# Kernel optimization log

Measured on AMD Instinct MI355X. Metric: run time of the kernel, lower is better.

The kernel has to match this reference:

```python
import jax, jax.numpy as jnp
import numpy as np

DIM = 256
HEADS = 8
DIM_HEAD = 32
AGENT = 6
WIN = 7


def _relative_position_index(L, Wh, Ww):
    coords = np.stack(np.meshgrid(np.arange(L), np.arange(Wh), np.arange(Ww), indexing='ij'))
    cf = coords.reshape(3, -1)                      # (3, N)
    rel = cf[:, :, None] - cf[:, None, :]           # (3, N, N)
    rel = rel.transpose(1, 2, 0).astype(np.int64)   # (N, N, 3)
    rel[..., 0] += L - 1
    rel[..., 1] += Wh - 1
    rel[..., 2] += Ww - 1
    rel[..., 0] *= (2 * Wh - 1) * (2 * Ww - 1)
    rel[..., 1] *= 2 * Ww - 1
    return rel.sum(-1)                              # (N, N)


def setup_inputs() -> dict:
    key = jax.random.key(0)
    k1, k2, k3, k4, k5 = jax.random.split(key, 5)
    B, X, Y = 2, 8, 8
    x = jax.random.normal(k1, (B, AGENT, X, Y, WIN, WIN, DIM), dtype=jnp.float32)
    mask = jax.random.randint(k2, (B, X, Y, WIN, WIN, 1, AGENT), 0, 2, dtype=jnp.int32)
    w_qkv = jax.random.normal(k3, (3 * DIM, DIM), dtype=jnp.float32) * 0.02
    w_out = jax.random.normal(k4, (DIM, DIM), dtype=jnp.float32) * 0.02
    n_bias = (2 * AGENT - 1) * (2 * WIN - 1) * (2 * WIN - 1)
    bias_table = jax.random.normal(k5, (n_bias, HEADS), dtype=jnp.float32) * 0.02
    return {"x": x, "mask": mask, "w_qkv": w_qkv, "w_out": w_out, "bias_table": bias_table}


def reference(x, mask, w_qkv, w_out, bias_table):
    B, L, X, Y, W1, W2, C = x.shape
    h, dh = HEADS, DIM_HEAD
    N = L * W1 * W2
    scale = dh ** -0.5

    # 'b l x y w1 w2 d -> (b x y) (l w1 w2) d'
    xr = jnp.transpose(x, (0, 2, 3, 1, 4, 5, 6)).reshape(B * X * Y, N, C)

    qkv = jnp.einsum('bnc,ec->bne', xr, w_qkv)      # (Bw, N, 3C)
    q, k, v = jnp.split(qkv, 3, axis=-1)
    def to_heads(t):
        return jnp.transpose(t.reshape(B * X * Y, N, h, dh), (0, 2, 1, 3))
    q, k, v = to_heads(q) * scale, to_heads(k), to_heads(v)

    sim = jnp.einsum('bhid,bhjd->bhij', q, k)       # (Bw, h, N, N)

    rel_idx = jnp.asarray(_relative_position_index(L, W1, W2))
    bias = bias_table[rel_idx]                      # (N, N, h)
    sim = sim + jnp.transpose(bias, (2, 0, 1))[None]

    # 'b x y w1 w2 e l -> (b x y) e (l w1 w2)'
    m = jnp.transpose(mask, (0, 1, 2, 5, 6, 3, 4)).reshape(B * X * Y, 1, N)
    sim = jnp.where(m[:, :, None, :] == 0, jnp.float32(-1e9), sim)

    attn = jax.nn.softmax(sim, axis=-1)
    out = jnp.einsum('bhij,bhjd->bhid', attn, v)    # (Bw, h, N, dh)

    # 'b h (l w1 w2) d -> b l w1 w2 (h d)'
    out = jnp.transpose(out, (0, 2, 1, 3)).reshape(B * X * Y, L, W1, W2, C)
    out = jnp.einsum('blwvc,ec->blwve', out, w_out)

    # '(b x y) l w1 w2 d -> b l x y w1 w2 d'
    out = out.reshape(B, X, Y, L, W1, W2, C)
    return jnp.transpose(out, (0, 3, 1, 2, 4, 5, 6))
```

## Files before the change

### kernel.cpp

```cpp
#include <hip/hip_runtime.h>
#include <hip/hip_bf16.h>

#define DIM 256
#define HEADS 8
#define DH 32
#define AGENT 6
#define WIN 7
#define NTOK 294
#define BWIN 128
#define SCALE 0.17677669529663687f
#define LOG2E 1.4426950408889634f
#define TP 19
#define QSTR 40
#define PSTR 320

typedef __hip_bfloat16 bf16;
typedef __attribute__((ext_vector_type(8))) short s16x8;
typedef __attribute__((ext_vector_type(4))) float f32x4;
typedef __attribute__((ext_vector_type(4))) unsigned int u32x4;

#if __has_builtin(__builtin_amdgcn_exp2f)
#define EXP2(x) __builtin_amdgcn_exp2f(x)
#else
#define EXP2(x) exp2f(x)
#endif

__device__ __forceinline__ float bfv(unsigned short u){ return __uint_as_float(((unsigned int)u) << 16); }
__device__ __forceinline__ unsigned short f2bu(float f){
    bf16 b = __float2bfloat16(f); return *reinterpret_cast<unsigned short*>(&b);
}
__device__ __forceinline__ float rdf(const void* p, size_t idx, int isf32) {
    return isf32 ? ((const float*)p)[idx] : bfv(((const unsigned short*)p)[idx]);
}

__device__ __forceinline__ int vtswz(int d, int cByte) {
    return (d * (PSTR * 2) + cByte) ^ (((d >> 1) & 7) << 4);
}

__device__ __forceinline__ void gll16(const void* gp, void* lp) {
    __builtin_amdgcn_global_load_lds(
        (const __attribute__((address_space(1))) unsigned int*)gp,
        (__attribute__((address_space(3))) unsigned int*)lp, 16, 0, 0);
}

__device__ __forceinline__ int detect_flag(const unsigned short* __restrict__ xraw,
                                           int* sflag, int nthreads) {
    if (threadIdx.x == 0) *sflag = 0;
    __syncthreads();
    int bad = 0;
    for (int i = threadIdx.x; i < 8192; i += nthreads) {
        float v = bfv(xraw[i]);
        if (!(fabsf(v) <= 1e10f)) bad = 1;
    }
    if (bad) atomicOr(sflag, 1);
    __syncthreads();
    return *sflag;
}

__global__ __launch_bounds__(256) void prep_kernel(
    const unsigned short* __restrict__ xraw,
    const void* __restrict__ wq, const void* __restrict__ wo, const void* __restrict__ bt,
    unsigned short* __restrict__ Wq, unsigned short* __restrict__ Wo,
    unsigned short* __restrict__ biasB) {
    __shared__ int sflag;
    const int isf32 = detect_flag(xraw, &sflag, 256);
    const int bid = blockIdx.x;
    if (bid < 722) {
        int idx = bid * 256 + threadIdx.x;
        int lane = idx & 63; int t = idx >> 6;
        int jt = t % TP; t /= TP; int it = t % TP; int h = t / TP;
        int i = it * 16 + (lane & 15);
        int g = lane >> 4;
        ushort4 v;
        unsigned short* vp = (unsigned short*)&v;
        #pragma unroll
        for (int r = 0; r < 4; r++) {
            int j = jt * 16 + g * 4 + r;
            float val = 0.f;
            if (i < NTOK && j < NTOK) {
                int li = i / 49, ri = i - li * 49, w1i = ri / 7, w2i = ri - w1i * 7;
                int lj = j / 49, rj = j - lj * 49, w1j = rj / 7, w2j = rj - w1j * 7;
                int rel = (li - lj + AGENT - 1) * 169 + (w1i - w1j + WIN - 1) * 13 + (w2i - w2j + WIN - 1);
                val = rdf(bt, (size_t)rel * HEADS + h, isf32) * LOG2E;
            }
            vp[r] = f2bu(val);
        }
        ((ushort4*)biasB)[idx] = v;
    } else {
        int c = (bid - 722) * 256 + threadIdx.x;
        const void* src; unsigned short* dst; size_t off;
        if (c < 24576) { src = wq; dst = Wq; off = (size_t)c * 8; }
        else           { src = wo; dst = Wo; off = (size_t)(c - 24576) * 8; }
        if (isf32) {
            const float4* s4 = (const float4*)((const float*)src + off);
            float4 v0 = s4[0], v1 = s4[1];
            s16x8 u;
            u[0] = (short)f2bu(v0.x); u[1] = (short)f2bu(v0.y); u[2] = (short)f2bu(v0.z); u[3] = (short)f2bu(v0.w);
            u[4] = (short)f2bu(v1.x); u[5] = (short)f2bu(v1.y); u[6] = (short)f2bu(v1.z); u[7] = (short)f2bu(v1.w);
            *(s16x8*)(dst + off) = u;
        } else {
            *(uint4*)(dst + off) = *(const uint4*)((const unsigned short*)src + off);
        }
    }
}

__device__ __forceinline__ void stage64_g(const unsigned short* __restrict__ g,
                                          unsigned short* lds, size_t rowBase) {
    const int lane = threadIdx.x & 63, wv = threadIdx.x >> 6;
    const int sub = lane >> 5;
    const int colB = (lane & 31) << 4;
    #pragma unroll
    for (int k = 0; k < 8; k++) {
        const int rr = (wv * 8 + k) * 2 + sub;
        const int cg = colB ^ ((rr & 7) << 4);
        gll16((const char*)g + (rowBase + (size_t)rr) * 512 + cg,
              lds + (size_t)(wv * 8 + k) * 512);
    }
}

__device__ __forceinline__ void stage64_f(const float* __restrict__ g,
                                          unsigned short* lds, size_t rowBase) {
    const int tid = threadIdx.x;
    #pragma unroll
    for (int k = 0; k < 8; k++) {
        int ch = k * 256 + tid;
        int rr = ch >> 5;
        int cB = (ch & 31) << 4;
        int cg = cB ^ ((rr & 7) << 4);
        const f32x4* s4 = (const f32x4*)(g + (rowBase + (size_t)rr) * 256 + (cg >> 1));
        f32x4 v0 = __builtin_nontemporal_load(s4);
        f32x4 v1 = __builtin_nontemporal_load(s4 + 1);
        s16x8 u;
        u[0] = (short)f2bu(v0[0]); u[1] = (short)f2bu(v0[1]); u[2] = (short)f2bu(v0[2]); u[3] = (short)f2bu(v0[3]);
        u[4] = (short)f2bu(v1[0]); u[5] = (short)f2bu(v1[1]); u[6] = (short)f2bu(v1[2]); u[7] = (short)f2bu(v1[3]);
        *(s16x8*)(lds + (size_t)rr * 256 + (cB >> 1)) = u;
    }
}

__global__ __launch_bounds__(256) void qkv_mfma(
    const void* __restrict__ xin, const unsigned short* __restrict__ Wq,
    bf16* __restrict__ Q, bf16* __restrict__ K, bf16* __restrict__ V) {
    __shared__ unsigned short As[64 * 256];
    __shared__ unsigned short Bs[64 * 256];
    __shared__ int sflag;
    const int isf32 = detect_flag((const unsigned short*)xin, &sflag, 256);
    const size_t mBase = (size_t)blockIdx.x * 64;
    if (isf32) stage64_f((const float*)xin, As, mBase);
    else       stage64_g((const unsigned short*)xin, As, mBase);
    const int tid = threadIdx.x;
    const int wave = tid >> 6, lane = tid & 63;
    const int li = lane & 15, g = lane >> 4;
    const int wm = wave & 1, wn = wave >> 1;
    unsigned int rowOff[2][4];
    #pragma unroll
    for (int mi = 0; mi < 2; mi++)
        #pragma unroll
        for (int r = 0; r < 4; r++) {
            unsigned int m = (unsigned int)mBase + wm * 32 + mi * 16 + g * 4 + r;
            unsigned int w2 = m % 7u, t1 = m / 7u;
            unsigned int w1 = t1 % 7u, t2 = t1 / 7u;
            unsigned int yy = t2 & 7u, t3 = t2 >> 3;
            unsigned int xx = t3 & 7u, t4 = t3 >> 3;
            unsigned int l = t4 % 6u, b = t4 / 6u;
            unsigned int bw = (b << 6) | (xx << 3) | yy;
            unsigned int n = l * 49u + w1 * 7u + w2;
            rowOff[mi][r] = bw * 75264u + n * 32u;
        }
    const int koX = (li & 7) * 8;
    for (int pc = 0; pc < 12; pc++) {
        __syncthreads();
        stage64_g(Wq, Bs, (size_t)pc * 64);
        __syncthreads();
        f32x4 acc[2][2];
        #pragma unroll
        for (int mi = 0; mi < 2; mi++)
            #pragma unroll
            for (int ni = 0; ni < 2; ni++) acc[mi][ni] = (f32x4){0.f, 0.f, 0.f, 0.f};
        #pragma unroll
        for (int kc = 0; kc < 8; kc++) {
            const int ko = (kc * 32 + g * 8) ^ koX;
            s16x8 a0 = *(const s16x8*)&As[(wm * 32 + li) * 256 + ko];
            s16x8 a1 = *(const s16x8*)&As[(wm * 32 + 16 + li) * 256 + ko];
            s16x8 b0 = *(const s16x8*)&Bs[(wn * 32 + li) * 256 + ko];
            s16x8 b1 = *(const s16x8*)&Bs[(wn * 32 + 16 + li) * 256 + ko];
            acc[0][0] = __builtin_amdgcn_mfma_f32_16x16x32_bf16(a0, b0, acc[0][0], 0, 0, 0);
            acc[0][1] = __builtin_amdgcn_mfma_f32_16x16x32_bf16(a0, b1, acc[0][1], 0, 0, 0);
            acc[1][0] = __builtin_amdgcn_mfma_f32_16x16x32_bf16(a1, b0, acc[1][0], 0, 0, 0);
            acc[1][1] = __builtin_amdgcn_mfma_f32_16x16x32_bf16(a1, b1, acc[1][1], 0, 0, 0);
        }
        const int p = pc >> 2;
        bf16* dst = (p == 0) ? Q : (p == 1) ? K : V;
        const float sc = (p == 0) ? (SCALE * LOG2E) : 1.0f;
        const unsigned int hoff = ((pc & 3) * 2 + wn) * 9408u;
        #pragma unroll
        for (int ni = 0; ni < 2; ni++) {
            const unsigned int d = ni * 16 + li;
            #pragma unroll
            for (int mi = 0; mi < 2; mi++)
                #pragma unroll
                for (int r = 0; r < 4; r++)
                    dst[(size_t)(rowOff[mi][r] + hoff + d)] =
                        __float2bfloat16(acc[mi][ni][r] * sc);
        }
    }
}

__global__ __launch_bounds__(512, 2) void attn_mfma(
    const bf16* __restrict__ Q, const bf16* __restrict__ K, const bf16* __restrict__ V,
    const unsigned short* __restrict__ biasB, const int* __restrict__ mask,
    bf16* __restrict__ AT) {
    __shared__ unsigned short Qs[304 * QSTR];
    __shared__ unsigned short Ks[304 * QSTR];
    __shared__ unsigned short Vt[32 * PSTR];
    __shared__ int ms[320];
    const int tid = threadIdx.x;
    const int bw = blockIdx.x >> 3, h = blockIdx.x & 7;
    const size_t base = ((size_t)bw * HEADS + h) * NTOK * DH;
    const unsigned int* Qg = (const unsigned int*)(Q + base);
    const unsigned int* Kg = (const unsigned int*)(K + base);
    const unsigned int* Vg = (const unsigned int*)(V + base);
    char* VtB = (char*)Vt;
    for (int gg = tid; gg < NTOK * DH / 2; gg += 512) {
        int r = gg >> 4, d2 = (gg & 15) * 2;
        unsigned int uq = __builtin_nontemporal_load(&Qg[gg]);
        unsigned int uk = __builtin_nontemporal_load(&Kg[gg]);
        unsigned int uv = __builtin_nontemporal_load(&Vg[gg]);
        *(unsigned int*)&Qs[r * QSTR + d2] = uq;
        *(unsigned int*)&Ks[r * QSTR + d2] = uk;
        *(unsigned short*)(VtB + vtswz(d2,     r * 2)) = (unsigned short)(uv & 0xffffu);
        *(unsigned short*)(VtB + vtswz(d2 + 1, r * 2)) = (unsigned short)(uv >> 16);
    }
    for (int e = NTOK * QSTR + tid; e < 304 * QSTR; e += 512) { Qs[e] = 0; Ks[e] = 0; }
    for (int idx = tid; idx < 32 * (PSTR - NTOK); idx += 512) {
        int d = idx / (PSTR - NTOK), c = NTOK + idx % (PSTR - NTOK);
        *(unsigned short*)(VtB + vtswz(d, c * 2)) = 0;
    }
    for (int j = tid; j < 320; j += 512) {
        int mv = 0;
        if (j < NTOK) { int a = j / 49, jr = j - a * 49; mv = mask[((size_t)bw * 49 + jr) * AGENT + a]; }
        ms[j] = mv;
    }
    __syncthreads();
    const int wave = tid >> 6, lane = tid & 63;
    const int li = lane & 15, g = lane >> 4;
    unsigned int mb0 = 0, mb1 = 0, mb2 = 0;
    for (int jt = 0; jt < TP; jt++)
        for (int r = 0; r < 4; r++) {
            int j = jt * 16 + g * 4 + r;
            if (j < NTOK && ms[j]) {
                int bit = jt * 4 + r;
                if (bit < 32) mb0 |= (1u << bit);
                else if (bit < 64) mb1 |= (1u << (bit - 32));
                else mb2 |= (1u << (bit - 64));
            }
        }
    const ushort4* bb = (const ushort4*)biasB + (size_t)h * TP * TP * 64;
    const int sAg = li + ((lane & 16) << 1);
    const int sBg = sAg + 16;
    const bool hiSel = (lane >= 32);
    for (int it = wave; it < TP; it += 8) {
        const s16x8 bq = *(const s16x8*)&Qs[(it * 16 + li) * QSTR + g * 8];
        f32x4 s[TP];
        __builtin_amdgcn_s_setprio(1);
        #pragma unroll
        for (int jt = 0; jt < TP; jt++) {
            ushort4 bv = bb[(it * TP + jt) * 64 + lane];
            f32x4 c = {bfv(bv.x), bfv(bv.y), bfv(bv.z), bfv(bv.w)};
            s16x8 ak = *(const s16x8*)&Ks[(jt * 16 + li) * QSTR + g * 8];
            s[jt] = __builtin_amdgcn_mfma_f32_16x16x32_bf16(ak, bq, c, 0, 0, 0);
        }
        __builtin_amdgcn_s_setprio(0);
        float mx = -INFINITY;
        #pragma unroll
        for (int jt = 0; jt < TP; jt++)
            #pragma unroll
            for (int r = 0; r < 4; r++) {
                int bit = jt * 4 + r;
                unsigned int w = (bit < 32) ? mb0 : (bit < 64) ? mb1 : mb2;
                float sv = ((w >> (bit & 31)) & 1u) ? s[jt][r] : -1e9f;
                if (jt == TP - 1 && g * 4 + r >= 6) sv = -INFINITY;
                s[jt][r] = sv;
                mx = fmaxf(mx, sv);
            }
        mx = fmaxf(mx, __shfl_xor(mx, 16));
        mx = fmaxf(mx, __shfl_xor(mx, 32));
        float sum = 0.f;
        unsigned int p0[TP], p1[TP];
        #pragma unroll
        for (int jt = 0; jt < TP; jt++) {
            float e0 = EXP2(s[jt][0] - mx);
            float e1 = EXP2(s[jt][1] - mx);
            float e2 = EXP2(s[jt][2] - mx);
            float e3 = EXP2(s[jt][3] - mx);
            sum += (e0 + e1) + (e2 + e3);
            unsigned int lo, hi;
            asm("v_cvt_pk_bf16_f32 %0, %1, %2" : "=v"(lo) : "v"(e0), "v"(e1));
            asm("v_cvt_pk_bf16_f32 %0, %1, %2" : "=v"(hi) : "v"(e2), "v"(e3));
            p0[jt] = lo; p1[jt] = hi;
        }
        sum += __shfl_xor(sum, 16);
        sum += __shfl_xor(sum, 32);
        const float inv = 1.0f / sum;
        f32x4 o0 = {0.f, 0.f, 0.f, 0.f}, o1 = {0.f, 0.f, 0.f, 0.f};
        #pragma unroll
        for (int kc = 0; kc < 10; kc++) {
            unsigned int a0q = __shfl(p0[2 * kc], sAg);
            unsigned int b0q = __shfl(p1[2 * kc], sAg);
            unsigned int c0q = __shfl(p0[2 * kc], sBg);
            unsigned int d0q = __shfl(p1[2 * kc], sBg);
            unsigned int a1q = 0, b1q = 0, c1q = 0, d1q = 0;
            if (2 * kc + 1 < TP) {
                a1q = __shfl(p0[2 * kc + 1], sAg);
                b1q = __shfl(p1[2 * kc + 1], sAg);
                c1q = __shfl(p0[2 * kc + 1], sBg);
                d1q = __shfl(p1[2 * kc + 1], sBg);
            }
            u32x4 w;
            w[0] = hiSel ? a1q : a0q;
            w[1] = hiSel ? b1q : b0q;
            w[2] = hiSel ? c1q : c0q;
            w[3] = hiSel ? d1q : d0q;
            s16x8 ap = __builtin_bit_cast(s16x8, w);
            s16x8 b0 = *(const s16x8*)(VtB + vtswz(li,      (kc * 32 + g * 8) * 2));
            s16x8 b1 = *(const s16x8*)(VtB + vtswz(li + 16, (kc * 32 + g * 8) * 2));
            __builtin_amdgcn_s_setprio(1);
            o0 = __builtin_amdgcn_mfma_f32_16x16x32_bf16(ap, b0, o0, 0, 0, 0);
            o1 = __builtin_amdgcn_mfma_f32_16x16x32_bf16(ap, b1, o1, 0, 0, 0);
            __builtin_amdgcn_s_setprio(0);
        }
        #pragma unroll
        for (int r = 0; r < 4; r++) {
            float iv = __shfl(inv, g * 4 + r);
            int i = it * 16 + g * 4 + r;
            if (i < NTOK) {
                size_t ob = ((size_t)bw * NTOK + i) * DIM + h * DH;
                AT[ob + li]      = __float2bfloat16(o0[r] * iv);
                AT[ob + 16 + li] = __float2bfloat16(o1[r] * iv);
            }
        }
    }
}

__global__ __launch_bounds__(256) void proj_mfma(
    const bf16* __restrict__ AT, const unsigned short* __restrict__ Wo,
    float* __restrict__ out) {
    __shared__ unsigned short As[64 * 256];
    __shared__ unsigned short Bs[64 * 256];
    const size_t mBase = (size_t)blockIdx.x * 64;
    stage64_g((const unsigned short*)AT, As, mBase);
    const int tid = threadIdx.x;
    const int wave = tid >> 6, lane = tid & 63;
    const int li = lane & 15, g = lane >> 4;
    const int wm = wave & 1, wn = wave >> 1;
    unsigned int offO[2][4];
    #pragma unroll
    for (int mi = 0; mi < 2; mi++)
        #pragma unroll
        for (int r = 0; r < 4; r++) {
            unsigned int m = (unsigned int)mBase + wm * 32 + mi * 16 + g * 4 + r;
            unsigned int bw = m / 294u, n = m - bw * 294u;
            unsigned int b = bw >> 6, xx = (bw >> 3) & 7u, yy = bw & 7u;
            unsigned int l = n / 49u, rr = n - l * 49u, w1 = rr / 7u, w2 = rr - w1 * 7u;
            offO[mi][r] = ((((((b * 6u + l) * 8u + xx) * 8u + yy) * 7u + w1) * 7u) + w2) * 256u;
        }
    const int koX = (li & 7) * 8;
    for (int ec = 0; ec < 4; ec++) {
        __syncthreads();
        stage64_g(Wo, Bs, (size_t)ec * 64);
        __syncthreads();
        f32x4 acc[2][2];
        #pragma unroll
        for (int mi = 0; mi < 2; mi++)
            #pragma unroll
            for (int ni = 0; ni < 2; ni++) acc[mi][ni] = (f32x4){0.f, 0.f, 0.f, 0.f};
        #pragma unroll
        for (int kc = 0; kc < 8; kc++) {
            const int ko = (kc * 32 + g * 8) ^ koX;
            s16x8 a0 = *(const s16x8*)&As[(wm * 32 + li) * 256 + ko];
            s16x8 a1 = *(const s16x8*)&As[(wm * 32 + 16 + li) * 256 + ko];
            s16x8 b0 = *(const s16x8*)&Bs[(wn * 32 + li) * 256 + ko];
            s16x8 b1 = *(const s16x8*)&Bs[(wn * 32 + 16 + li) * 256 + ko];
            acc[0][0] = __builtin_amdgcn_mfma_f32_16x16x32_bf16(a0, b0, acc[0][0], 0, 0, 0);
            acc[0][1] = __builtin_amdgcn_mfma_f32_16x16x32_bf16(a0, b1, acc[0][1], 0, 0, 0);
            acc[1][0] = __builtin_amdgcn_mfma_f32_16x16x32_bf16(a1, b0, acc[1][0], 0, 0, 0);
            acc[1][1] = __builtin_amdgcn_mfma_f32_16x16x32_bf16(a1, b1, acc[1][1], 0, 0, 0);
        }
        #pragma unroll
        for (int ni = 0; ni < 2; ni++) {
            const unsigned int e = ec * 64 + wn * 32 + ni * 16 + li;
            #pragma unroll
            for (int mi = 0; mi < 2; mi++)
                #pragma unroll
                for (int r = 0; r < 4; r++)
                    __builtin_nontemporal_store(acc[mi][ni][r],
                        &out[(size_t)(offO[mi][r] + e)]);
        }
    }
}

extern "C" void kernel_launch(void* const* d_in, const int* in_sizes, int n_in,
                              void* d_out, int out_size, void* d_ws, size_t ws_size,
                              hipStream_t stream) {
    const long long SZ_X = 9633792, SZ_M = 37632, SZ_WQ = 196608, SZ_WO = 65536, SZ_BT = 14872;
    const void* x = d_in[0]; const void* maskp = d_in[1]; const void* wqkv = d_in[2];
    const void* wout = d_in[3]; const void* btab = d_in[4];
    for (int i = 0; i < n_in; i++) {
        long long s = in_sizes[i];
        if (s == SZ_X) x = d_in[i];
        else if (s == SZ_M) maskp = d_in[i];
        else if (s == SZ_WQ) wqkv = d_in[i];
        else if (s == SZ_WO) wout = d_in[i];
        else if (s == SZ_BT) btab = d_in[i];
    }
    const int* mask = (const int*)maskp;
    float* out = (float*)d_out;
    const size_t SZ = (size_t)BWIN * NTOK * DIM;
    bf16* Q  = (bf16*)d_ws;
    bf16* K  = Q + SZ;
    bf16* V  = K + SZ;
    bf16* AT = V + SZ;
    unsigned short* biasB = (unsigned short*)(AT + SZ);
    const size_t NBB = (size_t)HEADS * TP * TP * 64 * 4;
    unsigned short* Wq = biasB + NBB;
    unsigned short* Wo = Wq + 196608;
    prep_kernel<<<dim3(850), dim3(256), 0, stream>>>(
        (const unsigned short*)x, wqkv, wout, btab, Wq, Wo, biasB);
    qkv_mfma<<<dim3(588), dim3(256), 0, stream>>>(x, Wq, Q, K, V);
    attn_mfma<<<dim3(BWIN * HEADS), dim3(512), 0, stream>>>(Q, K, V, biasB, mask, AT);
    proj_mfma<<<dim3(588), dim3(256), 0, stream>>>(AT, Wo, out);
}
```

Before: 214.6 us.

## Double-buffer weight tiles in QKV/proj GEMMs and split softmax reductions

The QKV and output-projection GEMMs now stage the weight matrix in 32-row chunks into two LDS buffers. The next chunk is prefetched while the current one feeds the MFMAs, which removes one barrier per chunk and overlaps weight loads with compute. The cost is half as many MFMAs per barrier and twice as many iterations. The softmax max and sum reductions in the attention kernel are also split across four independent accumulators to shorten their dependency chains.

```diff
diff --git a/kernel.cpp b/kernel.cpp
--- a/kernel.cpp
+++ b/kernel.cpp
@@ -118,6 +118,20 @@
     }
 }
 
+__device__ __forceinline__ void stage32_g(const unsigned short* __restrict__ g,
+                                          unsigned short* lds, size_t rowBase) {
+    const int tid = threadIdx.x;
+    #pragma unroll
+    for (int k = 0; k < 4; k++) {
+        int ch = k * 256 + tid;
+        int rr = ch >> 5;
+        int cB = (ch & 31) << 4;
+        int cg = cB ^ ((rr & 7) << 4);
+        gll16((const char*)g + (rowBase + (size_t)rr) * 512 + cg,
+              lds + (size_t)ch * 8);
+    }
+}
+
 __device__ __forceinline__ void stage64_f(const float* __restrict__ g,
                                           unsigned short* lds, size_t rowBase) {
     const int tid = threadIdx.x;
@@ -141,12 +155,13 @@
     const void* __restrict__ xin, const unsigned short* __restrict__ Wq,
     bf16* __restrict__ Q, bf16* __restrict__ K, bf16* __restrict__ V) {
     __shared__ unsigned short As[64 * 256];
-    __shared__ unsigned short Bs[64 * 256];
+    __shared__ unsigned short Bs[2][32 * 256];
     __shared__ int sflag;
     const int isf32 = detect_flag((const unsigned short*)xin, &sflag, 256);
     const size_t mBase = (size_t)blockIdx.x * 64;
     if (isf32) stage64_f((const float*)xin, As, mBase);
     else       stage64_g((const unsigned short*)xin, As, mBase);
+    stage32_g(Wq, Bs[0], 0);
     const int tid = threadIdx.x;
     const int wave = tid >> 6, lane = tid & 63;
     const int li = lane & 15, g = lane >> 4;
@@ -167,40 +182,30 @@
             rowOff[mi][r] = bw * 75264u + n * 32u;
         }
     const int koX = (li & 7) * 8;
-    for (int pc = 0; pc < 12; pc++) {
+    const unsigned int d = wn * 16 + li;
+    for (int c = 0; c < 24; c++) {
+        const unsigned short* Bcur = Bs[c & 1];
+        unsigned short* Bnxt = Bs[(c & 1) ^ 1];
         __syncthreads();
-        stage64_g(Wq, Bs, (size_t)pc * 64);
-        __syncthreads();
-        f32x4 acc[2][2];
-        #pragma unroll
-        for (int mi = 0; mi < 2; mi++)
-            #pragma unroll
-            for (int ni = 0; ni < 2; ni++) acc[mi][ni] = (f32x4){0.f, 0.f, 0.f, 0.f};
+        if (c + 1 < 24) stage32_g(Wq, Bnxt, (size_t)(c + 1) * 32);
+        f32x4 acc0 = {0.f,0.f,0.f,0.f}, acc1 = {0.f,0.f,0.f,0.f};
         #pragma unroll
         for (int kc = 0; kc < 8; kc++) {
             const int ko = (kc * 32 + g * 8) ^ koX;
             s16x8 a0 = *(const s16x8*)&As[(wm * 32 + li) * 256 + ko];
             s16x8 a1 = *(const s16x8*)&As[(wm * 32 + 16 + li) * 256 + ko];
-            s16x8 b0 = *(const s16x8*)&Bs[(wn * 32 + li) * 256 + ko];
-            s16x8 b1 = *(const s16x8*)&Bs[(wn * 32 + 16 + li) * 256 + ko];
-            acc[0][0] = __builtin_amdgcn_mfma_f32_16x16x32_bf16(a0, b0, acc[0][0], 0, 0, 0);
-            acc[0][1] = __builtin_amdgcn_mfma_f32_16x16x32_bf16(a0, b1, acc[0][1], 0, 0, 0);
-            acc[1][0] = __builtin_amdgcn_mfma_f32_16x16x32_bf16(a1, b0, acc[1][0], 0, 0, 0);
-            acc[1][1] = __builtin_amdgcn_mfma_f32_16x16x32_bf16(a1, b1, acc[1][1], 0, 0, 0);
-        }
-        const int p = pc >> 2;
+            s16x8 b0 = *(const s16x8*)&Bcur[(wn * 16 + li) * 256 + ko];
+            acc0 = __builtin_amdgcn_mfma_f32_16x16x32_bf16(a0, b0, acc0, 0, 0, 0);
+            acc1 = __builtin_amdgcn_mfma_f32_16x16x32_bf16(a1, b0, acc1, 0, 0, 0);
+        }
+        const int p = c >> 3;
         bf16* dst = (p == 0) ? Q : (p == 1) ? K : V;
         const float sc = (p == 0) ? (SCALE * LOG2E) : 1.0f;
-        const unsigned int hoff = ((pc & 3) * 2 + wn) * 9408u;
-        #pragma unroll
-        for (int ni = 0; ni < 2; ni++) {
-            const unsigned int d = ni * 16 + li;
-            #pragma unroll
-            for (int mi = 0; mi < 2; mi++)
-                #pragma unroll
-                for (int r = 0; r < 4; r++)
-                    dst[(size_t)(rowOff[mi][r] + hoff + d)] =
-                        __float2bfloat16(acc[mi][ni][r] * sc);
+        const unsigned int hoff = (c & 7) * 9408u;
+        #pragma unroll
+        for (int r = 0; r < 4; r++) {
+            dst[(size_t)(rowOff[0][r] + hoff + d)] = __float2bfloat16(acc0[r] * sc);
+            dst[(size_t)(rowOff[1][r] + hoff + d)] = __float2bfloat16(acc1[r] * sc);
         }
     }
 }
@@ -270,21 +275,29 @@
             s[jt] = __builtin_amdgcn_mfma_f32_16x16x32_bf16(ak, bq, c, 0, 0, 0);
         }
         __builtin_amdgcn_s_setprio(0);
-        float mx = -INFINITY;
-        #pragma unroll
-        for (int jt = 0; jt < TP; jt++)
+        float mA = -3e38f, mB = -3e38f, mC = -3e38f, mD = -3e38f;
+        #pragma unroll
+        for (int jt = 0; jt < TP; jt++) {
+            float sv[4];
             #pragma unroll
             for (int r = 0; r < 4; r++) {
                 int bit = jt * 4 + r;
                 unsigned int w = (bit < 32) ? mb0 : (bit < 64) ? mb1 : mb2;
-                float sv = ((w >> (bit & 31)) & 1u) ? s[jt][r] : -1e9f;
-                if (jt == TP - 1 && g * 4 + r >= 6) sv = -INFINITY;
-                s[jt][r] = sv;
-                mx = fmaxf(mx, sv);
+                float x = ((w >> (bit & 31)) & 1u) ? s[jt][r] : -1e9f;
+                if (jt == TP - 1 && g * 4 + r >= 6) x = -INFINITY;
+                sv[r] = x;
+                s[jt][r] = x;
             }
+            float mj = fmaxf(fmaxf(sv[0], sv[1]), fmaxf(sv[2], sv[3]));
+            if ((jt & 3) == 0)      mA = fmaxf(mA, mj);
+            else if ((jt & 3) == 1) mB = fmaxf(mB, mj);
+            else if ((jt & 3) == 2) mC = fmaxf(mC, mj);
+            else                    mD = fmaxf(mD, mj);
+        }
+        float mx = fmaxf(fmaxf(mA, mB), fmaxf(mC, mD));
         mx = fmaxf(mx, __shfl_xor(mx, 16));
         mx = fmaxf(mx, __shfl_xor(mx, 32));
-        float sum = 0.f;
+        float sSA = 0.f, sSB = 0.f, sSC = 0.f, sSD = 0.f;
         unsigned int p0[TP], p1[TP];
         #pragma unroll
         for (int jt = 0; jt < TP; jt++) {
@@ -292,12 +305,17 @@
             float e1 = EXP2(s[jt][1] - mx);
             float e2 = EXP2(s[jt][2] - mx);
             float e3 = EXP2(s[jt][3] - mx);
-            sum += (e0 + e1) + (e2 + e3);
+            float s4 = (e0 + e1) + (e2 + e3);
+            if ((jt & 3) == 0)      sSA += s4;
+            else if ((jt & 3) == 1) sSB += s4;
+            else if ((jt & 3) == 2) sSC += s4;
+            else                    sSD += s4;
             unsigned int lo, hi;
             asm("v_cvt_pk_bf16_f32 %0, %1, %2" : "=v"(lo) : "v"(e0), "v"(e1));
             asm("v_cvt_pk_bf16_f32 %0, %1, %2" : "=v"(hi) : "v"(e2), "v"(e3));
             p0[jt] = lo; p1[jt] = hi;
         }
+        float sum = (sSA + sSB) + (sSC + sSD);
         sum += __shfl_xor(sum, 16);
         sum += __shfl_xor(sum, 32);
         const float inv = 1.0f / sum;
@@ -345,9 +363,10 @@
     const bf16* __restrict__ AT, const unsigned short* __restrict__ Wo,
     float* __restrict__ out) {
     __shared__ unsigned short As[64 * 256];
-    __shared__ unsigned short Bs[64 * 256];
+    __shared__ unsigned short Bs[2][32 * 256];
     const size_t mBase = (size_t)blockIdx.x * 64;
     stage64_g((const unsigned short*)AT, As, mBase);
+    stage32_g(Wo, Bs[0], 0);
     const int tid = threadIdx.x;
     const int wave = tid >> 6, lane = tid & 63;
     const int li = lane & 15, g = lane >> 4;
@@ -364,36 +383,26 @@
             offO[mi][r] = ((((((b * 6u + l) * 8u + xx) * 8u + yy) * 7u + w1) * 7u) + w2) * 256u;
         }
     const int koX = (li & 7) * 8;
-    for (int ec = 0; ec < 4; ec++) {
+    for (int c = 0; c < 8; c++) {
+        const unsigned short* Bcur = Bs[c & 1];
+        unsigned short* Bnxt = Bs[(c & 1) ^ 1];
         __syncthreads();
-        stage64_g(Wo, Bs, (size_t)ec * 64);
-        __syncthreads();
-        f32x4 acc[2][2];
-        #pragma unroll
-        for (int mi = 0; mi < 2; mi++)
-            #pragma unroll
-            for (int ni = 0; ni < 2; ni++) acc[mi][ni] = (f32x4){0.f, 0.f, 0.f, 0.f};
+        if (c + 1 < 8) stage32_g(Wo, Bnxt, (size_t)(c + 1) * 32);
+        f32x4 acc0 = {0.f,0.f,0.f,0.f}, acc1 = {0.f,0.f,0.f,0.f};
         #pragma unroll
         for (int kc = 0; kc < 8; kc++) {
             const int ko = (kc * 32 + g * 8) ^ koX;
             s16x8 a0 = *(const s16x8*)&As[(wm * 32 + li) * 256 + ko];
             s16x8 a1 = *(const s16x8*)&As[(wm * 32 + 16 + li) * 256 + ko];
-            s16x8 b0 = *(const s16x8*)&Bs[(wn * 32 + li) * 256 + ko];
-            s16x8 b1 = *(const s16x8*)&Bs[(wn * 32 + 16 + li) * 256 + ko];
-            acc[0][0] = __builtin_amdgcn_mfma_f32_16x16x32_bf16(a0, b0, acc[0][0], 0, 0, 0);
-            acc[0][1] = __builtin_amdgcn_mfma_f32_16x16x32_bf16(a0, b1, acc[0][1], 0, 0, 0);
-            acc[1][0] = __builtin_amdgcn_mfma_f32_16x16x32_bf16(a1, b0, acc[1][0], 0, 0, 0);
-            acc[1][1] = __builtin_amdgcn_mfma_f32_16x16x32_bf16(a1, b1, acc[1][1], 0, 0, 0);
-        }
-        #pragma unroll
-        for (int ni = 0; ni < 2; ni++) {
-            const unsigned int e = ec * 64 + wn * 32 + ni * 16 + li;
-            #pragma unroll
-            for (int mi = 0; mi < 2; mi++)
-                #pragma unroll
-                for (int r = 0; r < 4; r++)
-                    __builtin_nontemporal_store(acc[mi][ni][r],
-                        &out[(size_t)(offO[mi][r] + e)]);
+            s16x8 b0 = *(const s16x8*)&Bcur[(wn * 16 + li) * 256 + ko];
+            acc0 = __builtin_amdgcn_mfma_f32_16x16x32_bf16(a0, b0, acc0, 0, 0, 0);
+            acc1 = __builtin_amdgcn_mfma_f32_16x16x32_bf16(a1, b0, acc1, 0, 0, 0);
+        }
+        const unsigned int e = c * 32 + wn * 16 + li;
+        #pragma unroll
+        for (int r = 0; r < 4; r++) {
+            __builtin_nontemporal_store(acc0[r], &out[(size_t)(offO[0][r] + e)]);
+            __builtin_nontemporal_store(acc1[r], &out[(size_t)(offO[1][r] + e)]);
         }
     }
 }
```

Result: slower. 232.4 us (+8.3%).

## Use permlane swaps for P relayout, fp32 bias, and mask inside exp

Applied to the files above, without the earlier changes.

Replaces the ds_bpermute-based shuffles that rearrange the softmax probabilities into MFMA A-operand layout with v_permlane32/16_swap cross-lane swaps. Stores the relative-position bias as fp32 so it feeds the MFMA accumulator directly without bf16 unpacking. Applies the mask by zeroing exponentials instead of writing -1e9 into scores before the max. This cuts LDS-path shuffle traffic and VALU select work, but doubles bias memory reads. An all-masked row would now divide by zero instead of giving a uniform distribution.

```diff
diff --git a/kernel.cpp b/kernel.cpp
--- a/kernel.cpp
+++ b/kernel.cpp
@@ -33,6 +33,13 @@
     return isf32 ? ((const float*)p)[idx] : bfv(((const unsigned short*)p)[idx]);
 }
 
+__device__ __forceinline__ void pl32(unsigned int &a, unsigned int &b){
+    asm("v_permlane32_swap_b32 %0, %1" : "+v"(a), "+v"(b));
+}
+__device__ __forceinline__ void pl16(unsigned int &a, unsigned int &b){
+    asm("v_permlane16_swap_b32 %0, %1" : "+v"(a), "+v"(b));
+}
+
 __device__ __forceinline__ int vtswz(int d, int cByte) {
     return (d * (PSTR * 2) + cByte) ^ (((d >> 1) & 7) << 4);
 }
@@ -61,7 +68,7 @@
     const unsigned short* __restrict__ xraw,
     const void* __restrict__ wq, const void* __restrict__ wo, const void* __restrict__ bt,
     unsigned short* __restrict__ Wq, unsigned short* __restrict__ Wo,
-    unsigned short* __restrict__ biasB) {
+    float* __restrict__ biasB) {
     __shared__ int sflag;
     const int isf32 = detect_flag(xraw, &sflag, 256);
     const int bid = blockIdx.x;
@@ -71,8 +78,7 @@
         int jt = t % TP; t /= TP; int it = t % TP; int h = t / TP;
         int i = it * 16 + (lane & 15);
         int g = lane >> 4;
-        ushort4 v;
-        unsigned short* vp = (unsigned short*)&v;
+        f32x4 v;
         #pragma unroll
         for (int r = 0; r < 4; r++) {
             int j = jt * 16 + g * 4 + r;
@@ -83,9 +89,9 @@
                 int rel = (li - lj + AGENT - 1) * 169 + (w1i - w1j + WIN - 1) * 13 + (w2i - w2j + WIN - 1);
                 val = rdf(bt, (size_t)rel * HEADS + h, isf32) * LOG2E;
             }
-            vp[r] = f2bu(val);
-        }
-        ((ushort4*)biasB)[idx] = v;
+            v[r] = val;
+        }
+        ((f32x4*)biasB)[idx] = v;
     } else {
         int c = (bid - 722) * 256 + threadIdx.x;
         const void* src; unsigned short* dst; size_t off;
@@ -207,7 +213,7 @@
 
 __global__ __launch_bounds__(512, 2) void attn_mfma(
     const bf16* __restrict__ Q, const bf16* __restrict__ K, const bf16* __restrict__ V,
-    const unsigned short* __restrict__ biasB, const int* __restrict__ mask,
+    const float* __restrict__ biasB, const int* __restrict__ mask,
     bf16* __restrict__ AT) {
     __shared__ unsigned short Qs[304 * QSTR];
     __shared__ unsigned short Ks[304 * QSTR];
@@ -254,9 +260,7 @@
                 else mb2 |= (1u << (bit - 64));
             }
         }
-    const ushort4* bb = (const ushort4*)biasB + (size_t)h * TP * TP * 64;
-    const int sAg = li + ((lane & 16) << 1);
-    const int sBg = sAg + 16;
+    const f32x4* bb = (const f32x4*)biasB + (size_t)h * TP * TP * 64;
     const bool hiSel = (lane >= 32);
     for (int it = wave; it < TP; it += 8) {
         const s16x8 bq = *(const s16x8*)&Qs[(it * 16 + li) * QSTR + g * 8];
@@ -264,34 +268,31 @@
         __builtin_amdgcn_s_setprio(1);
         #pragma unroll
         for (int jt = 0; jt < TP; jt++) {
-            ushort4 bv = bb[(it * TP + jt) * 64 + lane];
-            f32x4 c = {bfv(bv.x), bfv(bv.y), bfv(bv.z), bfv(bv.w)};
+            f32x4 c = bb[(it * TP + jt) * 64 + lane];
             s16x8 ak = *(const s16x8*)&Ks[(jt * 16 + li) * QSTR + g * 8];
             s[jt] = __builtin_amdgcn_mfma_f32_16x16x32_bf16(ak, bq, c, 0, 0, 0);
         }
         __builtin_amdgcn_s_setprio(0);
-        float mx = -INFINITY;
-        #pragma unroll
-        for (int jt = 0; jt < TP; jt++)
-            #pragma unroll
-            for (int r = 0; r < 4; r++) {
-                int bit = jt * 4 + r;
-                unsigned int w = (bit < 32) ? mb0 : (bit < 64) ? mb1 : mb2;
-                float sv = ((w >> (bit & 31)) & 1u) ? s[jt][r] : -1e9f;
-                if (jt == TP - 1 && g * 4 + r >= 6) sv = -INFINITY;
-                s[jt][r] = sv;
-                mx = fmaxf(mx, sv);
-            }
+        float m0 = -3e38f, m1 = -3e38f;
+        #pragma unroll
+        for (int jt = 0; jt < TP; jt++) {
+            m0 = fmaxf(m0, fmaxf(s[jt][0], s[jt][1]));
+            m1 = fmaxf(m1, fmaxf(s[jt][2], s[jt][3]));
+        }
+        float mx = fmaxf(m0, m1);
         mx = fmaxf(mx, __shfl_xor(mx, 16));
         mx = fmaxf(mx, __shfl_xor(mx, 32));
         float sum = 0.f;
         unsigned int p0[TP], p1[TP];
         #pragma unroll
         for (int jt = 0; jt < TP; jt++) {
-            float e0 = EXP2(s[jt][0] - mx);
-            float e1 = EXP2(s[jt][1] - mx);
-            float e2 = EXP2(s[jt][2] - mx);
-            float e3 = EXP2(s[jt][3] - mx);
+            const int bit = jt * 4;
+            const unsigned int w = (bit < 32) ? mb0 : (bit < 64) ? mb1 : mb2;
+            const int bs = bit & 31;
+            float e0 = ((w >> bs) & 1u)       ? EXP2(s[jt][0] - mx) : 0.f;
+            float e1 = ((w >> (bs + 1)) & 1u) ? EXP2(s[jt][1] - mx) : 0.f;
+            float e2 = ((w >> (bs + 2)) & 1u) ? EXP2(s[jt][2] - mx) : 0.f;
+            float e3 = ((w >> (bs + 3)) & 1u) ? EXP2(s[jt][3] - mx) : 0.f;
             sum += (e0 + e1) + (e2 + e3);
             unsigned int lo, hi;
             asm("v_cvt_pk_bf16_f32 %0, %1, %2" : "=v"(lo) : "v"(e0), "v"(e1));
@@ -304,22 +305,18 @@
         f32x4 o0 = {0.f, 0.f, 0.f, 0.f}, o1 = {0.f, 0.f, 0.f, 0.f};
         #pragma unroll
         for (int kc = 0; kc < 10; kc++) {
-            unsigned int a0q = __shfl(p0[2 * kc], sAg);
-            unsigned int b0q = __shfl(p1[2 * kc], sAg);
-            unsigned int c0q = __shfl(p0[2 * kc], sBg);
-            unsigned int d0q = __shfl(p1[2 * kc], sBg);
-            unsigned int a1q = 0, b1q = 0, c1q = 0, d1q = 0;
+            unsigned int xA0 = p0[2 * kc], xB0 = xA0; pl32(xA0, xB0); pl16(xA0, xB0);
+            unsigned int yA0 = p1[2 * kc], yB0 = yA0; pl32(yA0, yB0); pl16(yA0, yB0);
+            unsigned int xA1 = 0, xB1 = 0, yA1 = 0, yB1 = 0;
             if (2 * kc + 1 < TP) {
-                a1q = __shfl(p0[2 * kc + 1], sAg);
-                b1q = __shfl(p1[2 * kc + 1], sAg);
-                c1q = __shfl(p0[2 * kc + 1], sBg);
-                d1q = __shfl(p1[2 * kc + 1], sBg);
+                xA1 = p0[2 * kc + 1]; xB1 = xA1; pl32(xA1, xB1); pl16(xA1, xB1);
+                yA1 = p1[2 * kc + 1]; yB1 = yA1; pl32(yA1, yB1); pl16(yA1, yB1);
             }
             u32x4 w;
-            w[0] = hiSel ? a1q : a0q;
-            w[1] = hiSel ? b1q : b0q;
-            w[2] = hiSel ? c1q : c0q;
-            w[3] = hiSel ? d1q : d0q;
+            w[0] = hiSel ? xA1 : xA0;
+            w[1] = hiSel ? yA1 : yA0;
+            w[2] = hiSel ? xB1 : xB0;
+            w[3] = hiSel ? yB1 : yB0;
             s16x8 ap = __builtin_bit_cast(s16x8, w);
             s16x8 b0 = *(const s16x8*)(VtB + vtswz(li,      (kc * 32 + g * 8) * 2));
             s16x8 b1 = *(const s16x8*)(VtB + vtswz(li + 16, (kc * 32 + g * 8) * 2));
@@ -419,9 +416,9 @@
     bf16* K  = Q + SZ;
     bf16* V  = K + SZ;
     bf16* AT = V + SZ;
-    unsigned short* biasB = (unsigned short*)(AT + SZ);
-    const size_t NBB = (size_t)HEADS * TP * TP * 64 * 4;
-    unsigned short* Wq = biasB + NBB;
+    float* biasB = (float*)(AT + SZ);
+    const size_t NBBf = (size_t)HEADS * TP * TP * 64 * 4;
+    unsigned short* Wq = (unsigned short*)(biasB + NBBf);
     unsigned short* Wo = Wq + 196608;
     prep_kernel<<<dim3(850), dim3(256), 0, stream>>>(
         (const unsigned short*)x, wqkv, wout, btab, Wq, Wo, biasB);
```

New measurement: 219.0 us. +2.1%, slower.

## Double-buffer weight staging in QKV GEMM with A fragments kept in registers

Applied to the files above, without the earlier changes.

The QKV projection kernel now loads the A (activation) fragments from LDS into registers once. That frees the A buffer, which is reused as a second weight buffer. The next 64-row weight chunk is staged into the alternate buffer while the current chunk is consumed by MFMAs, so there is one barrier per iteration instead of two. This adds register pressure, since 16 vector registers of A fragments are held for the whole loop, and the overlap relies on the staging loads being issued before the MFMA work.

```diff
diff --git a/kernel.cpp b/kernel.cpp
--- a/kernel.cpp
+++ b/kernel.cpp
@@ -140,13 +140,14 @@
 __global__ __launch_bounds__(256) void qkv_mfma(
     const void* __restrict__ xin, const unsigned short* __restrict__ Wq,
     bf16* __restrict__ Q, bf16* __restrict__ K, bf16* __restrict__ V) {
-    __shared__ unsigned short As[64 * 256];
-    __shared__ unsigned short Bs[64 * 256];
+    __shared__ unsigned short P0[64 * 256];
+    __shared__ unsigned short P1[64 * 256];
     __shared__ int sflag;
     const int isf32 = detect_flag((const unsigned short*)xin, &sflag, 256);
     const size_t mBase = (size_t)blockIdx.x * 64;
-    if (isf32) stage64_f((const float*)xin, As, mBase);
-    else       stage64_g((const unsigned short*)xin, As, mBase);
+    if (isf32) stage64_f((const float*)xin, P1, mBase);
+    else       stage64_g((const unsigned short*)xin, P1, mBase);
+    stage64_g(Wq, P0, 0);
     const int tid = threadIdx.x;
     const int wave = tid >> 6, lane = tid & 63;
     const int li = lane & 15, g = lane >> 4;
@@ -167,10 +168,19 @@
             rowOff[mi][r] = bw * 75264u + n * 32u;
         }
     const int koX = (li & 7) * 8;
-    for (int pc = 0; pc < 12; pc++) {
-        __syncthreads();
-        stage64_g(Wq, Bs, (size_t)pc * 64);
-        __syncthreads();
+    __syncthreads();
+    s16x8 a0r[8], a1r[8];
+    #pragma unroll
+    for (int kc = 0; kc < 8; kc++) {
+        const int ko = (kc * 32 + g * 8) ^ koX;
+        a0r[kc] = *(const s16x8*)&P1[(wm * 32 + li) * 256 + ko];
+        a1r[kc] = *(const s16x8*)&P1[(wm * 32 + 16 + li) * 256 + ko];
+    }
+    __syncthreads();
+    for (int c = 0; c < 12; c++) {
+        const unsigned short* Bc = (c & 1) ? P1 : P0;
+        unsigned short* Bn = (c & 1) ? P0 : P1;
+        if (c + 1 < 12) stage64_g(Wq, Bn, (size_t)(c + 1) * 64);
         f32x4 acc[2][2];
         #pragma unroll
         for (int mi = 0; mi < 2; mi++)
@@ -179,19 +189,17 @@
         #pragma unroll
         for (int kc = 0; kc < 8; kc++) {
             const int ko = (kc * 32 + g * 8) ^ koX;
-            s16x8 a0 = *(const s16x8*)&As[(wm * 32 + li) * 256 + ko];
-            s16x8 a1 = *(const s16x8*)&As[(wm * 32 + 16 + li) * 256 + ko];
-            s16x8 b0 = *(const s16x8*)&Bs[(wn * 32 + li) * 256 + ko];
-            s16x8 b1 = *(const s16x8*)&Bs[(wn * 32 + 16 + li) * 256 + ko];
-            acc[0][0] = __builtin_amdgcn_mfma_f32_16x16x32_bf16(a0, b0, acc[0][0], 0, 0, 0);
-            acc[0][1] = __builtin_amdgcn_mfma_f32_16x16x32_bf16(a0, b1, acc[0][1], 0, 0, 0);
-            acc[1][0] = __builtin_amdgcn_mfma_f32_16x16x32_bf16(a1, b0, acc[1][0], 0, 0, 0);
-            acc[1][1] = __builtin_amdgcn_mfma_f32_16x16x32_bf16(a1, b1, acc[1][1], 0, 0, 0);
-        }
-        const int p = pc >> 2;
+            s16x8 b0 = *(const s16x8*)&Bc[(wn * 32 + li) * 256 + ko];
+            s16x8 b1 = *(const s16x8*)&Bc[(wn * 32 + 16 + li) * 256 + ko];
+            acc[0][0] = __builtin_amdgcn_mfma_f32_16x16x32_bf16(a0r[kc], b0, acc[0][0], 0, 0, 0);
+            acc[0][1] = __builtin_amdgcn_mfma_f32_16x16x32_bf16(a0r[kc], b1, acc[0][1], 0, 0, 0);
+            acc[1][0] = __builtin_amdgcn_mfma_f32_16x16x32_bf16(a1r[kc], b0, acc[1][0], 0, 0, 0);
+            acc[1][1] = __builtin_amdgcn_mfma_f32_16x16x32_bf16(a1r[kc], b1, acc[1][1], 0, 0, 0);
+        }
+        const int p = c >> 2;
         bf16* dst = (p == 0) ? Q : (p == 1) ? K : V;
         const float sc = (p == 0) ? (SCALE * LOG2E) : 1.0f;
-        const unsigned int hoff = ((pc & 3) * 2 + wn) * 9408u;
+        const unsigned int hoff = ((c & 3) * 2 + wn) * 9408u;
         #pragma unroll
         for (int ni = 0; ni < 2; ni++) {
             const unsigned int d = ni * 16 + li;
@@ -202,6 +210,7 @@
                     dst[(size_t)(rowOff[mi][r] + hoff + d)] =
                         __float2bfloat16(acc[mi][ni][r] * sc);
         }
+        __syncthreads();
     }
 }
 
```

After: 209.1 us. 2.5% less time.
